# Performance work log

Hardware: AMD Instinct MI355X
Metric: run time of the kernel (lower is better)

Reference implementation:

```python
import jax, jax.numpy as jnp
import numpy as np

B, S, H, V, T, L = 32, 128, 1024, 32000, 100, 4
SD = 0.02


def setup_inputs() -> dict:
    key = jax.random.key(0)
    ks = jax.random.split(key, 20)
    f = jnp.float32
    return {
        "encoder_outputs": jax.random.normal(ks[0], (B, S, H), f),
        "encoder_hidden": jax.random.normal(ks[1], (L, B, H), f),
        "target_tensor": jax.random.randint(ks[2], (B, T), 0, V, dtype=jnp.int32),
        "emb": jax.random.normal(ks[3], (V, H), f) * SD,
        "w_ih0": jax.random.normal(ks[4], (3 * H, 2 * H), f) * SD,
        "w_hh0": jax.random.normal(ks[5], (3 * H, H), f) * SD,
        "b_ih0": jnp.zeros((3 * H,), f),
        "b_hh0": jnp.zeros((3 * H,), f),
        "w_ih": jax.random.normal(ks[6], (L - 1, 3 * H, H), f) * SD,
        "w_hh": jax.random.normal(ks[7], (L - 1, 3 * H, H), f) * SD,
        "b_ih": jnp.zeros((L - 1, 3 * H), f),
        "b_hh": jnp.zeros((L - 1, 3 * H), f),
        "out_w": jax.random.normal(ks[8], (V, H), f) * SD,
        "out_b": jnp.zeros((V,), f),
        "l1_w": jax.random.normal(ks[9], (3, 2 * H), f) * SD,
        "l1_b": jnp.zeros((3,), f),
        "l2_w": jax.random.normal(ks[10], (1, 3), f) * SD,
        "l2_b": jnp.zeros((1,), f),
    }


def _gru_cell(x, h, w_ih, w_hh, b_ih, b_hh):
    # PyTorch GRUCell math
    gi = x @ w_ih.T + b_ih          # [B, 3H]
    gh = h @ w_hh.T + b_hh          # [B, 3H]
    i_r, i_z, i_n = jnp.split(gi, 3, axis=-1)
    h_r, h_z, h_n = jnp.split(gh, 3, axis=-1)
    r = jax.nn.sigmoid(i_r + h_r)
    z = jax.nn.sigmoid(i_z + h_z)
    n = jnp.tanh(i_n + r * h_n)
    return (1.0 - z) * n + z * h


def reference(encoder_outputs, encoder_hidden, target_tensor, emb,
              w_ih0, w_hh0, b_ih0, b_hh0, w_ih, w_hh, b_ih, b_hh,
              out_w, out_b, l1_w, l1_b, l2_w, l2_b):
    b, h = encoder_hidden.shape[1], encoder_hidden.shape[2]
    enc_h = encoder_hidden[0]  # [B, H] 'updated_encoder_hidden'
    # teacher forcing: step 0 uses input 0, step i uses target[:, i-1]
    inputs = jnp.concatenate(
        [jnp.zeros((b, 1), target_tensor.dtype), target_tensor[:, :T - 1]],
        axis=1).T  # [T, B]

    def step(hidden, inp_t):
        # a[:] = hidden[0][-1] -> broadcast last batch row of layer-0 hidden
        a = jnp.broadcast_to(hidden[0, -1], (b, h))
        enc = jnp.concatenate([a, enc_h], axis=1)          # [B, 2H]
        s = (enc @ l1_w.T + l1_b) @ l2_w.T + l2_b          # [B, 1]
        scores = jax.nn.softmax(s, axis=0)                 # softmax over batch dim
        C = jnp.sum(enc_h * scores, axis=0)                # [H]
        e = jax.nn.relu(emb[inp_t])                        # [B, H]
        x = jnp.concatenate([e, jnp.broadcast_to(C, (b, h))], axis=-1)  # [B, 2H]
        h0 = _gru_cell(x, hidden[0], w_ih0, w_hh0, b_ih0, b_hh0)
        hs = [h0]
        xl = h0
        for l in range(L - 1):
            hl = _gru_cell(xl, hidden[l + 1], w_ih[l], w_hh[l], b_ih[l], b_hh[l])
            hs.append(hl)
            xl = hl
        logits = xl @ out_w.T + out_b                      # [B, V]
        return jnp.stack(hs), (logits, scores)

    hidden_fin, (logits, scores) = jax.lax.scan(step, encoder_hidden, inputs)
    dec_out = jax.nn.log_softmax(jnp.transpose(logits, (1, 0, 2)), axis=-1)  # [B, T, V]
    return dec_out, hidden_fin, scores[-1]
```

## Files before the change

### kernel.cpp

```cpp
#include <hip/hip_runtime.h>
#include <hip/hip_bf16.h>
#include <math.h>

#define B_ 32
#define H_ 1024
#define V_ 32000
#define T_ 100
#define L_ 4
#define TB_ (T_*B_)
#define N3H (3*H_)
#define NBLK 224
#define L0BLK 32
#define FSTRIDE 16
#define NVT (V_/128)

typedef __attribute__((ext_vector_type(8))) short bf16x8;
typedef __attribute__((ext_vector_type(4))) float f32x4;
typedef __attribute__((ext_vector_type(4))) unsigned short u16x4;
typedef __attribute__((ext_vector_type(8))) unsigned short u16x8;

__device__ inline unsigned short f2bf(float f) {
    union { float f; unsigned u; } v; v.f = f;
    unsigned r = v.u + 0x7fff + ((v.u >> 16) & 1);
    return (unsigned short)(r >> 16);
}
__device__ inline float bf2f(unsigned short u) {
    union { unsigned u; float f; } v; v.u = ((unsigned)u) << 16; return v.f;
}

__device__ inline bf16x8 ld_h16(const unsigned short* p) {
    union { unsigned long long u[2]; bf16x8 v; } r;
    r.u[0] = __hip_atomic_load((const unsigned long long*)p,
                               __ATOMIC_RELAXED, __HIP_MEMORY_SCOPE_AGENT);
    r.u[1] = __hip_atomic_load((const unsigned long long*)(p + 4),
                               __ATOMIC_RELAXED, __HIP_MEMORY_SCOPE_AGENT);
    return r.v;
}
__device__ inline void st_h2(unsigned short* p, unsigned short v) {
    __hip_atomic_store(p, v, __ATOMIC_RELAXED, __HIP_MEMORY_SCOPE_AGENT);
}

__device__ inline void gload_lds16(const unsigned short* g, unsigned short* lds)
{
    __builtin_amdgcn_global_load_lds(
        (const __attribute__((address_space(1))) void*)g,
        (__attribute__((address_space(3))) void*)lds, 16, 0, 0);
}

__global__ __launch_bounds__(256) void convbf_kernel(
    const float* __restrict__ src, unsigned short* __restrict__ dst, int n4)
{
    for (int i = blockIdx.x * 256 + threadIdx.x; i < n4; i += gridDim.x * 256) {
        float4 v = ((const float4*)src)[i];
        u16x4 o; o.x = f2bf(v.x); o.y = f2bf(v.y); o.z = f2bf(v.z); o.w = f2bf(v.w);
        ((u16x4*)dst)[i] = o;
    }
}

__global__ __launch_bounds__(256) void embed_bf_kernel(
    const int* __restrict__ target, const float* __restrict__ emb,
    unsigned short* __restrict__ Ebf)
{
    int bid = blockIdx.x;
    int t = bid >> 5, b = bid & 31;
    int tok = (t == 0) ? 0 : target[b * T_ + (t - 1)];
    float4 v = ((const float4*)(emb + (size_t)tok * H_))[threadIdx.x];
    u16x4 o;
    o.x = f2bf(fmaxf(v.x, 0.f)); o.y = f2bf(fmaxf(v.y, 0.f));
    o.z = f2bf(fmaxf(v.z, 0.f)); o.w = f2bf(fmaxf(v.w, 0.f));
    ((u16x4*)(Ebf + (size_t)bid * H_))[threadIdx.x] = o;
}

__global__ __launch_bounds__(256) void attn_pre_kernel(
    const float* __restrict__ enc_h, const float* __restrict__ l1_w,
    const float* __restrict__ l1_b, const float* __restrict__ l2_w,
    float* __restrict__ Cout, float* __restrict__ scores)
{
    __shared__ float L1h[96];
    __shared__ float sc[32];
    int tid = threadIdx.x, wv = tid >> 6, lane = tid & 63;
    for (int d = wv; d < 96; d += 4) {
        int b = d / 3, g = d - 3 * b;
        const float4* wp = (const float4*)(l1_w + (size_t)g * 2 * H_ + H_);
        const float4* ep = (const float4*)(enc_h + (size_t)b * H_);
        float s = 0.f;
        for (int q = lane; q < 256; q += 64) {
            float4 w4 = wp[q], e4 = ep[q];
            s += w4.x * e4.x + w4.y * e4.y + w4.z * e4.z + w4.w * e4.w;
        }
        for (int o = 32; o > 0; o >>= 1) s += __shfl_down(s, o);
        if (lane == 0) L1h[d] = s;
    }
    __syncthreads();
    if (tid < 32) {
        float cb = 0.f;
        for (int g = 0; g < 3; ++g) cb += l2_w[g] * (L1h[tid * 3 + g] + l1_b[g]);
        sc[tid] = cb;
    }
    __syncthreads();
    if (tid == 0) {
        float m = sc[0];
        for (int b = 1; b < 32; ++b) m = fmaxf(m, sc[b]);
        float s = 0.f;
        for (int b = 0; b < 32; ++b) { float e = expf(sc[b] - m); sc[b] = e; s += e; }
        float inv = 1.f / s;
        for (int b = 0; b < 32; ++b) { sc[b] *= inv; scores[b] = sc[b]; }
    }
    __syncthreads();
    float4 c = make_float4(0.f, 0.f, 0.f, 0.f);
    for (int b = 0; b < 32; ++b) {
        float4 e = ((const float4*)(enc_h + (size_t)b * H_))[tid];
        float ww = sc[b];
        c.x += ww * e.x; c.y += ww * e.y; c.z += ww * e.z; c.w += ww * e.w;
    }
    ((float4*)Cout)[tid] = c;
}

__global__ __launch_bounds__(256) void wcc_kernel(
    const float* __restrict__ w_ih0, const float* __restrict__ C,
    float* __restrict__ wcC)
{
    int row = blockIdx.x * 4 + (threadIdx.x >> 6);
    int lane = threadIdx.x & 63;
    const float4* wp = (const float4*)(w_ih0 + (size_t)row * 2 * H_ + H_);
    const float4* cp = (const float4*)C;
    float s = 0.f;
    for (int q = lane; q < 256; q += 64) {
        float4 w4 = wp[q], c4 = cp[q];
        s += w4.x * c4.x + w4.y * c4.y + w4.z * c4.z + w4.w * c4.w;
    }
    for (int o = 32; o > 0; o >>= 1) s += __shfl_down(s, o);
    if (lane == 0) wcC[row] = s;
}

__global__ __launch_bounds__(256) void gemm_staged(
    const unsigned short* __restrict__ A, int lda,
    const unsigned short* __restrict__ Bb,
    const float* __restrict__ bias, int M, int outMode,
    void* __restrict__ outp, float2* __restrict__ P)
{
    __shared__ unsigned short Wt[128 * 64];
    __shared__ unsigned short Ht[128 * 64];
    __shared__ float2 smp[4][4][16];

    const int tid = threadIdx.x, wv = tid >> 6, lane = tid & 63;
    const int rlo = lane & 15, khw = lane >> 4;
    const int rch = lane >> 3, slot = lane & 7;
    const int rowB = blockIdx.y * 128, colB = blockIdx.x * 128;
    const int wrow0 = rowB + (wv >> 1) * 64;
    const int wcol0 = colB + (wv & 1) * 64;
    const int rA = (wv >> 1) * 64, cA = (wv & 1) * 64;

    f32x4 acc[4][4];
    #pragma unroll
    for (int i = 0; i < 4; ++i)
        #pragma unroll
        for (int j = 0; j < 4; ++j) acc[i][j] = (f32x4){0.f, 0.f, 0.f, 0.f};

    for (int k0 = 0; k0 < H_; k0 += 64) {
        #pragma unroll
        for (int j = 0; j < 4; ++j) {
            int q = wv * 4 + j;
            int row = q * 8 + rch;
            int ss = slot ^ (row & 7);
            gload_lds16(A + (size_t)(rowB + row) * lda + k0 + ss * 8,
                        Wt + (size_t)q * 512);
            gload_lds16(Bb + (size_t)(colB + row) * H_ + k0 + ss * 8,
                        Ht + (size_t)q * 512);
        }
        __syncthreads();

        const char* WtB = (const char*)Wt;
        const char* HtB = (const char*)Ht;
        #pragma unroll
        for (int kk = 0; kk < 2; ++kk) {
            bf16x8 af[4], bfr[4];
            #pragma unroll
            for (int ri = 0; ri < 4; ++ri) {
                int row = rA + ri * 16 + rlo;
                int ch = (kk * 4 + khw) ^ (row & 7);
                af[ri] = *(const bf16x8*)(WtB + row * 128 + ch * 16);
            }
            #pragma unroll
            for (int ci = 0; ci < 4; ++ci) {
                int col = cA + ci * 16 + rlo;
                int ch = (kk * 4 + khw) ^ (col & 7);
                bfr[ci] = *(const bf16x8*)(HtB + col * 128 + ch * 16);
            }
            #pragma unroll
            for (int ri = 0; ri < 4; ++ri)
                #pragma unroll
                for (int ci = 0; ci < 4; ++ci)
                    acc[ri][ci] = __builtin_amdgcn_mfma_f32_16x16x32_bf16(
                        af[ri], bfr[ci], acc[ri][ci], 0, 0, 0);
        }
        __syncthreads();
    }

    int rowoff = (lane >> 4) * 4;
    if (outMode == 0) {
        #pragma unroll
        for (int ri = 0; ri < 4; ++ri) {
            int row = wrow0 + ri * 16 + rowoff;
            float4 bs = *(const float4*)(bias + row);
            #pragma unroll
            for (int ci = 0; ci < 4; ++ci) {
                int col = wcol0 + ci * 16 + rlo;
                u16x4 o;
                o.x = f2bf(acc[ri][ci][0] + bs.x); o.y = f2bf(acc[ri][ci][1] + bs.y);
                o.z = f2bf(acc[ri][ci][2] + bs.z); o.w = f2bf(acc[ri][ci][3] + bs.w);
                *(u16x4*)((unsigned short*)outp + (size_t)col * M + row) = o;
            }
        }
        return;
    }

    float cm[4], cs[4];
    #pragma unroll
    for (int ci = 0; ci < 4; ++ci) { cm[ci] = -INFINITY; cs[ci] = 0.f; }
    unsigned short* Lbf = (unsigned short*)outp;
    #pragma unroll
    for (int ri = 0; ri < 4; ++ri) {
        int row = wrow0 + ri * 16 + rowoff;
        float4 bs = *(const float4*)(bias + row);
        #pragma unroll
        for (int ci = 0; ci < 4; ++ci) {
            int col = wcol0 + ci * 16 + rlo;
            float4 v;
            v.x = acc[ri][ci][0] + bs.x; v.y = acc[ri][ci][1] + bs.y;
            v.z = acc[ri][ci][2] + bs.z; v.w = acc[ri][ci][3] + bs.w;
            u16x4 o; o.x = f2bf(v.x); o.y = f2bf(v.y);
            o.z = f2bf(v.z); o.w = f2bf(v.w);
            *(u16x4*)(Lbf + (size_t)col * V_ + row) = o;
            float m4 = fmaxf(fmaxf(v.x, v.y), fmaxf(v.z, v.w));
            if (m4 > cm[ci]) { cs[ci] *= __expf(cm[ci] - m4); cm[ci] = m4; }
            cs[ci] += __expf(v.x - cm[ci]) + __expf(v.y - cm[ci])
                    + __expf(v.z - cm[ci]) + __expf(v.w - cm[ci]);
        }
    }
    #pragma unroll
    for (int ci = 0; ci < 4; ++ci) {
        #pragma unroll
        for (int off = 16; off <= 32; off <<= 1) {
            float om = __shfl_xor(cm[ci], off);
            float os = __shfl_xor(cs[ci], off);
            float mm = fmaxf(cm[ci], om);
            cs[ci] = cs[ci] * __expf(cm[ci] - mm) + os * __expf(om - mm);
            cm[ci] = mm;
        }
        if ((lane >> 4) == 0) smp[wv][ci][rlo] = make_float2(cm[ci], cs[ci]);
    }
    __syncthreads();
    if (tid < 128) {
        int c = tid >> 6, ci = (tid >> 4) & 3, rl = tid & 15;
        float2 a = smp[c][ci][rl], b = smp[c + 2][ci][rl];
        float mm = fmaxf(a.x, b.x);
        float ss = a.y * __expf(a.x - mm) + b.y * __expf(b.x - mm);
        int col = colB + c * 64 + ci * 16 + rl;
        P[(size_t)blockIdx.y * TB_ + col] = make_float2(mm, ss);
    }
}

__global__ __launch_bounds__(256) void lse_finish_kernel(
    const float2* __restrict__ P, float* __restrict__ lse)
{
    int col = blockIdx.x * 256 + threadIdx.x;
    if (col >= TB_) return;
    float M = -INFINITY, S = 0.f;
    for (int i = 0; i < NVT; ++i) {
        float2 p = P[(size_t)i * TB_ + col];
        float mm = fmaxf(M, p.x);
        S = S * __expf(M - mm) + p.y * __expf(p.x - mm);
        M = mm;
    }
    lse[col] = M + logf(S);
}

__global__ __launch_bounds__(256) void subtract_kernel(
    const unsigned short* __restrict__ Lbf, const float* __restrict__ lse,
    float* __restrict__ dout)
{
    int col = blockIdx.x;
    int t = col >> 5, b = col & 31;
    float l = lse[col];
    const u16x8* L = (const u16x8*)(Lbf + (size_t)col * V_);
    float4* o = (float4*)(dout + ((size_t)b * T_ + t) * V_);
    for (int i = threadIdx.x; i < V_ / 8; i += 256) {
        u16x8 x = L[i];
        float4 v0, v1;
        v0.x = bf2f(x[0]) - l; v0.y = bf2f(x[1]) - l;
        v0.z = bf2f(x[2]) - l; v0.w = bf2f(x[3]) - l;
        v1.x = bf2f(x[4]) - l; v1.y = bf2f(x[5]) - l;
        v1.z = bf2f(x[6]) - l; v1.w = bf2f(x[7]) - l;
        o[i * 2] = v0; o[i * 2 + 1] = v1;
    }
}

__device__ inline void grid_bar4(unsigned* flags, unsigned round)
{
    __syncthreads();
    if (threadIdx.x == 0) {
        asm volatile("s_waitcnt vmcnt(0)" ::: "memory");
        __hip_atomic_store(&flags[(size_t)blockIdx.x * FSTRIDE], round,
                           __ATOMIC_RELAXED, __HIP_MEMORY_SCOPE_AGENT);
    }
    int ok = (threadIdx.x >= NBLK) ? 1 : 0;
    while (true) {
        if (!ok)
            ok = (__hip_atomic_load(&flags[(size_t)threadIdx.x * FSTRIDE],
                                    __ATOMIC_RELAXED, __HIP_MEMORY_SCOPE_AGENT) >= round);
        if (__syncthreads_and(ok)) break;
        __builtin_amdgcn_s_sleep(2);
    }
}

__global__ __launch_bounds__(512, 1) void decode_kernel(
    const unsigned short* __restrict__ whh0_bf,
    const unsigned short* __restrict__ wih_bf,
    const unsigned short* __restrict__ whh_bf,
    const unsigned short* __restrict__ G0,
    const float* __restrict__ b_ih0, const float* __restrict__ b_hh0,
    const float* __restrict__ b_ih,  const float* __restrict__ b_hh,
    const float* __restrict__ enc_hidden,
    unsigned short* __restrict__ hbf,
    unsigned short* __restrict__ Hist,
    float* __restrict__ hid_out,
    unsigned* __restrict__ flags)
{
    __shared__ float sacc[6][4][16][34];
    const int tid = threadIdx.x;
    const int wv = tid >> 6, lane = tid & 63;
    const int rlo = lane & 15, klane = (lane >> 4) * 8;
    const int rowoff = (lane >> 4) * 4;
    const int bid = blockIdx.x;

    int layer, f0;
    if (bid < L0BLK) { layer = 0; f0 = bid << 5; }
    else { int r = bid - L0BLK; layer = 1 + (r >> 6); f0 = (r & 63) << 4; }

    const unsigned short* Wih_l = (layer >= 1) ? wih_bf + (size_t)(layer - 1) * N3H * H_ : nullptr;
    const unsigned short* Whh_l = (layer >= 1) ? whh_bf + (size_t)(layer - 1) * N3H * H_ : whh0_bf;

    const int kc = wv & 3, srcgrp = wv >> 2;

    bf16x8 wreg[3][8];
    int rgv[3];
    #pragma unroll
    for (int i = 0; i < 3; ++i) {
        int rg = srcgrp * 3 + i;
        rgv[i] = rg;
        int wrow; const unsigned short* Wm;
        if (layer == 0)      { wrow = (rg >> 1) * H_ + f0 + (rg & 1) * 16; Wm = Whh_l; }
        else if (rg < 3)     { wrow = rg * H_ + f0;        Wm = Wih_l; }
        else                 { wrow = (rg - 3) * H_ + f0;  Wm = Whh_l; }
        const unsigned short* p = Wm + (size_t)(wrow + rlo) * H_ + kc * 256 + klane;
        #pragma unroll
        for (int s = 0; s < 8; ++s) wreg[i][s] = *(const bf16x8*)(p + s * 32);
    }
    #pragma unroll
    for (int i = 0; i < 3; ++i)
        #pragma unroll
        for (int s = 0; s < 8; ++s)
            asm volatile("" : "+v"(wreg[i][s]));

    const float* bihp = (layer == 0) ? b_ih0 : b_ih + (size_t)(layer - 1) * N3H;
    const float* bhhp = (layer == 0) ? b_hh0 : b_hh + (size_t)(layer - 1) * N3H;
    int jj, eb0;
    float hold0, hold1 = 0.f;
    if (layer == 0) {
        jj = f0 + (tid & 31);
        eb0 = tid >> 5;
        hold0 = enc_hidden[(size_t)eb0 * H_ + jj];
        hold1 = enc_hidden[(size_t)(eb0 + 16) * H_ + jj];
    } else {
        jj = f0 + (tid & 15);
        eb0 = tid >> 4;
        hold0 = enc_hidden[(size_t)layer * B_ * H_ + (size_t)eb0 * H_ + jj];
    }
    const float bir = bihp[jj], biz = bihp[H_ + jj], bin_ = bihp[2 * H_ + jj];
    const float bhr = bhhp[jj], bhz = bhhp[H_ + jj], bhn = bhhp[2 * H_ + jj];

    const size_t BH = (size_t)B_ * H_;

    for (int c = 0; c < T_ + L_ - 1; ++c) {
        int t = c - layer;
        if (t >= 0 && t < T_) {
            int pw = t & 1, pr = pw ^ 1;
            const unsigned short* hown  = hbf + ((size_t)pr * L_ + layer) * BH;
            const unsigned short* hprev = (layer > 0)
                ? hbf + ((size_t)pw * L_ + (layer - 1)) * BH : nullptr;

            f32x4 acc[3][2];
            #pragma unroll
            for (int i = 0; i < 3; ++i) {
                acc[i][0] = (f32x4){0.f, 0.f, 0.f, 0.f};
                acc[i][1] = (f32x4){0.f, 0.f, 0.f, 0.f};
            }

            const unsigned short* hsrc = (layer == 0 || srcgrp == 1) ? hown : hprev;
            const unsigned short* hp = hsrc + (size_t)rlo * H_ + kc * 256 + klane;
            #pragma unroll
            for (int s = 0; s < 8; ++s) {
                bf16x8 b0 = ld_h16(hp + s * 32);
                bf16x8 b1 = ld_h16(hp + 16 * H_ + s * 32);
                #pragma unroll
                for (int i = 0; i < 3; ++i) {
                    acc[i][0] = __builtin_amdgcn_mfma_f32_16x16x32_bf16(wreg[i][s], b0, acc[i][0], 0, 0, 0);
                    acc[i][1] = __builtin_amdgcn_mfma_f32_16x16x32_bf16(wreg[i][s], b1, acc[i][1], 0, 0, 0);
                }
            }

            #pragma unroll
            for (int i = 0; i < 3; ++i)
                #pragma unroll
                for (int r = 0; r < 4; ++r) {
                    sacc[rgv[i]][kc][rowoff + r][rlo]      = acc[i][0][r];
                    sacc[rgv[i]][kc][rowoff + r][16 + rlo] = acc[i][1][r];
                }
            __syncthreads();

            if (layer > 0) {
                int f = tid & 15, b = tid >> 4;
                float ir = bir, iz = biz, in_ = bin_;
                float hr = bhr, hz = bhz, hn = bhn;
                #pragma unroll
                for (int k2 = 0; k2 < 4; ++k2) {
                    ir += sacc[0][k2][f][b]; iz += sacc[1][k2][f][b]; in_ += sacc[2][k2][f][b];
                    hr += sacc[3][k2][f][b]; hz += sacc[4][k2][f][b]; hn += sacc[5][k2][f][b];
                }
                float r = 1.f / (1.f + expf(-(ir + hr)));
                float z = 1.f / (1.f + expf(-(iz + hz)));
                float n = tanhf(in_ + r * hn);
                float hnew = (1.f - z) * n + z * hold0;
                hold0 = hnew;
                unsigned short hb16 = f2bf(hnew);
                st_h2(&hbf[((size_t)pw * L_ + layer) * BH + (size_t)b * H_ + jj], hb16);
                if (layer == L_ - 1) Hist[((size_t)t * B_ + b) * H_ + jj] = hb16;
                if (t == T_ - 1) hid_out[(size_t)layer * BH + (size_t)b * H_ + jj] = hnew;
            } else {
                int fi = tid & 31;
                int rghalf = fi >> 4, fr = fi & 15;
                {
                    int b = eb0;
                    const unsigned short* g0p = G0 + ((size_t)t * B_ + b) * N3H;
                    float ir = bf2f(g0p[jj]) + bir;
                    float iz = bf2f(g0p[H_ + jj]) + biz;
                    float in_ = bf2f(g0p[2 * H_ + jj]) + bin_;
                    float hr = bhr, hz = bhz, hn = bhn;
                    #pragma unroll
                    for (int k2 = 0; k2 < 4; ++k2) {
                        hr += sacc[rghalf][k2][fr][b];
                        hz += sacc[2 + rghalf][k2][fr][b];
                        hn += sacc[4 + rghalf][k2][fr][b];
                    }
                    float r = 1.f / (1.f + expf(-(ir + hr)));
                    float z = 1.f / (1.f + expf(-(iz + hz)));
                    float n = tanhf(in_ + r * hn);
                    float hnew = (1.f - z) * n + z * hold0;
                    hold0 = hnew;
                    st_h2(&hbf[((size_t)pw * L_) * BH + (size_t)b * H_ + jj], f2bf(hnew));
                    if (t == T_ - 1) hid_out[(size_t)b * H_ + jj] = hnew;
                }
                {
                    int b = eb0 + 16;
                    const unsigned short* g0p = G0 + ((size_t)t * B_ + b) * N3H;
                    float ir = bf2f(g0p[jj]) + bir;
                    float iz = bf2f(g0p[H_ + jj]) + biz;
                    float in_ = bf2f(g0p[2 * H_ + jj]) + bin_;
                    float hr = bhr, hz = bhz, hn = bhn;
                    #pragma unroll
                    for (int k2 = 0; k2 < 4; ++k2) {
                        hr += sacc[rghalf][k2][fr][b];
                        hz += sacc[2 + rghalf][k2][fr][b];
                        hn += sacc[4 + rghalf][k2][fr][b];
                    }
                    float r = 1.f / (1.f + expf(-(ir + hr)));
                    float z = 1.f / (1.f + expf(-(iz + hz)));
                    float n = tanhf(in_ + r * hn);
                    float hnew = (1.f - z) * n + z * hold1;
                    hold1 = hnew;
                    st_h2(&hbf[((size_t)pw * L_) * BH + (size_t)b * H_ + jj], f2bf(hnew));
                    if (t == T_ - 1) hid_out[(size_t)b * H_ + jj] = hnew;
                }
            }
        }
        grid_bar4(flags, (unsigned)(c + 1));
    }
}

__global__ __launch_bounds__(256) void logsoftmax_kernel(float* __restrict__ dout)
{
    __shared__ float red[256];
    float4* x4 = (float4*)(dout + (size_t)blockIdx.x * V_);
    const int N4 = V_ / 4;
    int tid = threadIdx.x;

    float m = -INFINITY, s = 0.f;
    for (int i = tid; i < N4; i += 256) {
        float4 v = x4[i];
        float m4 = fmaxf(fmaxf(v.x, v.y), fmaxf(v.z, v.w));
        if (m4 > m) { s *= expf(m - m4); m = m4; }
        s += expf(v.x - m) + expf(v.y - m) + expf(v.z - m) + expf(v.w - m);
    }
    red[tid] = m; __syncthreads();
    for (int o = 128; o > 0; o >>= 1) {
        if (tid < o) red[tid] = fmaxf(red[tid], red[tid + o]);
        __syncthreads();
    }
    float M = red[0]; __syncthreads();
    red[tid] = s * expf(m - M); __syncthreads();
    for (int o = 128; o > 0; o >>= 1) {
        if (tid < o) red[tid] += red[tid + o];
        __syncthreads();
    }
    float lse = M + logf(red[0]);

    for (int i = tid; i < N4; i += 256) {
        float4 v = x4[i];
        v.x -= lse; v.y -= lse; v.z -= lse; v.w -= lse;
        x4[i] = v;
    }
}

__global__ __launch_bounds__(256) void gemm_logits_f32(
    const unsigned short* __restrict__ A,
    const unsigned short* __restrict__ Bb,
    const float* __restrict__ bias, float* __restrict__ dout)
{
    __shared__ unsigned short Wt[128 * 64];
    __shared__ unsigned short Ht[128 * 64];
    const int tid = threadIdx.x, wv = tid >> 6, lane = tid & 63;
    const int rlo = lane & 15, khw = lane >> 4;
    const int rch = lane >> 3, slot = lane & 7;
    const int rowB = blockIdx.y * 128, colB = blockIdx.x * 128;
    const int wrow0 = rowB + (wv >> 1) * 64;
    const int wcol0 = colB + (wv & 1) * 64;
    const int rA = (wv >> 1) * 64, cA = (wv & 1) * 64;

    f32x4 acc[4][4];
    #pragma unroll
    for (int i = 0; i < 4; ++i)
        #pragma unroll
        for (int j = 0; j < 4; ++j) acc[i][j] = (f32x4){0.f, 0.f, 0.f, 0.f};

    for (int k0 = 0; k0 < H_; k0 += 64) {
        #pragma unroll
        for (int j = 0; j < 4; ++j) {
            int q = wv * 4 + j;
            int row = q * 8 + rch;
            int ss = slot ^ (row & 7);
            gload_lds16(A + (size_t)(rowB + row) * H_ + k0 + ss * 8, Wt + (size_t)q * 512);
            gload_lds16(Bb + (size_t)(colB + row) * H_ + k0 + ss * 8, Ht + (size_t)q * 512);
        }
        __syncthreads();
        const char* WtB = (const char*)Wt;
        const char* HtB = (const char*)Ht;
        #pragma unroll
        for (int kk = 0; kk < 2; ++kk) {
            bf16x8 af[4], bfr[4];
            #pragma unroll
            for (int ri = 0; ri < 4; ++ri) {
                int row = rA + ri * 16 + rlo;
                int ch = (kk * 4 + khw) ^ (row & 7);
                af[ri] = *(const bf16x8*)(WtB + row * 128 + ch * 16);
            }
            #pragma unroll
            for (int ci = 0; ci < 4; ++ci) {
                int col = cA + ci * 16 + rlo;
                int ch = (kk * 4 + khw) ^ (col & 7);
                bfr[ci] = *(const bf16x8*)(HtB + col * 128 + ch * 16);
            }
            #pragma unroll
            for (int ri = 0; ri < 4; ++ri)
                #pragma unroll
                for (int ci = 0; ci < 4; ++ci)
                    acc[ri][ci] = __builtin_amdgcn_mfma_f32_16x16x32_bf16(
                        af[ri], bfr[ci], acc[ri][ci], 0, 0, 0);
        }
        __syncthreads();
    }
    int rowoff = (lane >> 4) * 4;
    #pragma unroll
    for (int ri = 0; ri < 4; ++ri) {
        int row = wrow0 + ri * 16 + rowoff;
        float4 bs = *(const float4*)(bias + row);
        #pragma unroll
        for (int ci = 0; ci < 4; ++ci) {
            int col = wcol0 + ci * 16 + rlo;
            int tt = col >> 5, b = col & 31;
            float4 v;
            v.x = acc[ri][ci][0] + bs.x; v.y = acc[ri][ci][1] + bs.y;
            v.z = acc[ri][ci][2] + bs.z; v.w = acc[ri][ci][3] + bs.w;
            *(float4*)(dout + ((size_t)b * T_ + tt) * V_ + row) = v;
        }
    }
}

extern "C" void kernel_launch(void* const* d_in, const int* in_sizes, int n_in,
                              void* d_out, int out_size, void* d_ws, size_t ws_size,
                              hipStream_t stream)
{
    (void)in_sizes; (void)n_in; (void)out_size;

    const float* enc_hidden = (const float*)d_in[1];
    const int*   target     = (const int*)  d_in[2];
    const float* emb        = (const float*)d_in[3];
    const float* w_ih0      = (const float*)d_in[4];
    const float* w_hh0      = (const float*)d_in[5];
    const float* b_ih0      = (const float*)d_in[6];
    const float* b_hh0      = (const float*)d_in[7];
    const float* w_ih       = (const float*)d_in[8];
    const float* w_hh       = (const float*)d_in[9];
    const float* b_ih       = (const float*)d_in[10];
    const float* b_hh       = (const float*)d_in[11];
    const float* out_w      = (const float*)d_in[12];
    const float* out_b      = (const float*)d_in[13];
    const float* l1_w       = (const float*)d_in[14];
    const float* l1_b       = (const float*)d_in[15];
    const float* l2_w       = (const float*)d_in[16];
    float* out = (float*)d_out;

    char* w = (char*)d_ws;
    auto alloc = [&](size_t bytes) -> char* {
        char* p = w; w += (bytes + 255) & ~(size_t)255; return p;
    };
    unsigned short* whh0_bf = (unsigned short*)alloc((size_t)N3H * H_ * 2);
    unsigned short* wih_bf  = (unsigned short*)alloc((size_t)3 * N3H * H_ * 2);
    unsigned short* whh_bf  = (unsigned short*)alloc((size_t)3 * N3H * H_ * 2);
    unsigned short* Ebf     = (unsigned short*)alloc((size_t)TB_ * H_ * 2);
    unsigned short* G0      = (unsigned short*)alloc((size_t)TB_ * N3H * 2);
    unsigned short* Hist    = (unsigned short*)alloc((size_t)TB_ * H_ * 2);
    unsigned short* hbf     = (unsigned short*)alloc((size_t)2 * L_ * B_ * H_ * 2);
    float*          Cbuf    = (float*)alloc(H_ * 4);
    float*          scores  = (float*)alloc(256);
    float*          wcC     = (float*)alloc(N3H * 4);
    unsigned*       flags   = (unsigned*)alloc((size_t)NBLK * FSTRIDE * 4);
    float2*         Ppart   = (float2*)alloc((size_t)NVT * TB_ * 8);
    float*          lse     = (float*)alloc((size_t)TB_ * 4);

    size_t used = (size_t)(w - (char*)d_ws);
    unsigned short* wih0f_bf = nullptr;
    if (used + (size_t)N3H * 2 * H_ * 2 + 256 <= ws_size)
        wih0f_bf = (unsigned short*)alloc((size_t)N3H * 2 * H_ * 2);
    used = (size_t)(w - (char*)d_ws);
    unsigned short* outw_bf = nullptr;
    if (used + (size_t)V_ * H_ * 2 + 256 <= ws_size)
        outw_bf = (unsigned short*)alloc((size_t)V_ * H_ * 2);
    used = (size_t)(w - (char*)d_ws);
    unsigned short* Lbf = nullptr;
    if (used + (size_t)TB_ * V_ * 2 + 256 <= ws_size)
        Lbf = (unsigned short*)alloc((size_t)TB_ * V_ * 2);

    const size_t LBH = (size_t)L_ * B_ * H_;

    hipMemsetAsync(flags, 0, (size_t)NBLK * FSTRIDE * 4, stream);

    convbf_kernel<<<512, 256, 0, stream>>>(w_hh0, whh0_bf, N3H * H_ / 4);
    convbf_kernel<<<1024, 256, 0, stream>>>(w_ih, wih_bf, 3 * N3H * H_ / 4);
    convbf_kernel<<<1024, 256, 0, stream>>>(w_hh, whh_bf, 3 * N3H * H_ / 4);
    if (wih0f_bf)
        convbf_kernel<<<1024, 256, 0, stream>>>(w_ih0, wih0f_bf, N3H * 2 * H_ / 4);
    if (outw_bf)
        convbf_kernel<<<2048, 256, 0, stream>>>(out_w, outw_bf, V_ * H_ / 4);
    embed_bf_kernel<<<TB_, 256, 0, stream>>>(target, emb, Ebf);
    convbf_kernel<<<128, 256, 0, stream>>>(enc_hidden, hbf + LBH, (int)(LBH / 4));
    attn_pre_kernel<<<1, 256, 0, stream>>>(enc_hidden, l1_w, l1_b, l2_w, Cbuf, scores);
    wcc_kernel<<<N3H / 4, 256, 0, stream>>>(w_ih0, Cbuf, wcC);

    gemm_staged<<<dim3(TB_ / 128, N3H / 128), 256, 0, stream>>>(
        wih0f_bf, 2 * H_, Ebf, wcC, N3H, 0, G0, nullptr);

    decode_kernel<<<NBLK, 512, 0, stream>>>(
        whh0_bf, wih_bf, whh_bf, G0, b_ih0, b_hh0, b_ih, b_hh,
        enc_hidden, hbf, Hist, out + (size_t)B_ * T_ * V_, flags);

    if (outw_bf && Lbf) {
        gemm_staged<<<dim3(TB_ / 128, V_ / 128), 256, 0, stream>>>(
            outw_bf, H_, Hist, out_b, V_, 2, Lbf, Ppart);
        lse_finish_kernel<<<(TB_ + 255) / 256, 256, 0, stream>>>(Ppart, lse);
        subtract_kernel<<<TB_, 256, 0, stream>>>(Lbf, lse, out);
    } else if (outw_bf) {
        gemm_logits_f32<<<dim3(TB_ / 128, V_ / 128), 256, 0, stream>>>(
            outw_bf, Hist, out_b, out);
        logsoftmax_kernel<<<TB_, 256, 0, stream>>>(out);
    }

    hipMemcpyAsync(out + (size_t)B_ * T_ * V_ + LBH, scores, B_ * 4,
                   hipMemcpyDeviceToDevice, stream);
}
```

Measured before the change: 1.821 ms.

## Overlap output-projection GEMM with recurrent decode using extra worker blocks

```diff
diff --git a/kernel.cpp b/kernel.cpp
--- a/kernel.cpp
+++ b/kernel.cpp
@@ -11,6 +11,8 @@
 #define N3H (3*H_)
 #define NBLK 224
 #define L0BLK 32
+#define NWRK 200
+#define NCT  25
 #define FSTRIDE 16
 #define NVT (V_/128)
 
@@ -38,6 +40,9 @@
 }
 __device__ inline void st_h2(unsigned short* p, unsigned short v) {
     __hip_atomic_store(p, v, __ATOMIC_RELAXED, __HIP_MEMORY_SCOPE_AGENT);
+}
+__device__ inline unsigned ld_flag(const unsigned* p) {
+    return __hip_atomic_load(p, __ATOMIC_RELAXED, __HIP_MEMORY_SCOPE_AGENT);
 }
 
 __device__ inline void gload_lds16(const unsigned short* g, unsigned short* lds)
@@ -136,12 +141,11 @@
 __global__ __launch_bounds__(256) void gemm_staged(
     const unsigned short* __restrict__ A, int lda,
     const unsigned short* __restrict__ Bb,
-    const float* __restrict__ bias, int M, int outMode,
-    void* __restrict__ outp, float2* __restrict__ P)
+    const float* __restrict__ bias, int M,
+    unsigned short* __restrict__ outp)
 {
     __shared__ unsigned short Wt[128 * 64];
     __shared__ unsigned short Ht[128 * 64];
-    __shared__ float2 smp[4][4][16];
 
     const int tid = threadIdx.x, wv = tid >> 6, lane = tid & 63;
     const int rlo = lane & 15, khw = lane >> 4;
@@ -198,27 +202,6 @@
     }
 
     int rowoff = (lane >> 4) * 4;
-    if (outMode == 0) {
-        #pragma unroll
-        for (int ri = 0; ri < 4; ++ri) {
-            int row = wrow0 + ri * 16 + rowoff;
-            float4 bs = *(const float4*)(bias + row);
-            #pragma unroll
-            for (int ci = 0; ci < 4; ++ci) {
-                int col = wcol0 + ci * 16 + rlo;
-                u16x4 o;
-                o.x = f2bf(acc[ri][ci][0] + bs.x); o.y = f2bf(acc[ri][ci][1] + bs.y);
-                o.z = f2bf(acc[ri][ci][2] + bs.z); o.w = f2bf(acc[ri][ci][3] + bs.w);
-                *(u16x4*)((unsigned short*)outp + (size_t)col * M + row) = o;
-            }
-        }
-        return;
-    }
-
-    float cm[4], cs[4];
-    #pragma unroll
-    for (int ci = 0; ci < 4; ++ci) { cm[ci] = -INFINITY; cs[ci] = 0.f; }
-    unsigned short* Lbf = (unsigned short*)outp;
     #pragma unroll
     for (int ri = 0; ri < 4; ++ri) {
         int row = wrow0 + ri * 16 + rowoff;
@@ -226,38 +209,11 @@
         #pragma unroll
         for (int ci = 0; ci < 4; ++ci) {
             int col = wcol0 + ci * 16 + rlo;
-            float4 v;
-            v.x = acc[ri][ci][0] + bs.x; v.y = acc[ri][ci][1] + bs.y;
-            v.z = acc[ri][ci][2] + bs.z; v.w = acc[ri][ci][3] + bs.w;
-            u16x4 o; o.x = f2bf(v.x); o.y = f2bf(v.y);
-            o.z = f2bf(v.z); o.w = f2bf(v.w);
-            *(u16x4*)(Lbf + (size_t)col * V_ + row) = o;
-            float m4 = fmaxf(fmaxf(v.x, v.y), fmaxf(v.z, v.w));
-            if (m4 > cm[ci]) { cs[ci] *= __expf(cm[ci] - m4); cm[ci] = m4; }
-            cs[ci] += __expf(v.x - cm[ci]) + __expf(v.y - cm[ci])
-                    + __expf(v.z - cm[ci]) + __expf(v.w - cm[ci]);
-        }
-    }
-    #pragma unroll
-    for (int ci = 0; ci < 4; ++ci) {
-        #pragma unroll
-        for (int off = 16; off <= 32; off <<= 1) {
-            float om = __shfl_xor(cm[ci], off);
-            float os = __shfl_xor(cs[ci], off);
-            float mm = fmaxf(cm[ci], om);
-            cs[ci] = cs[ci] * __expf(cm[ci] - mm) + os * __expf(om - mm);
-            cm[ci] = mm;
-        }
-        if ((lane >> 4) == 0) smp[wv][ci][rlo] = make_float2(cm[ci], cs[ci]);
-    }
-    __syncthreads();
-    if (tid < 128) {
-        int c = tid >> 6, ci = (tid >> 4) & 3, rl = tid & 15;
-        float2 a = smp[c][ci][rl], b = smp[c + 2][ci][rl];
-        float mm = fmaxf(a.x, b.x);
-        float ss = a.y * __expf(a.x - mm) + b.y * __expf(b.x - mm);
-        int col = colB + c * 64 + ci * 16 + rl;
-        P[(size_t)blockIdx.y * TB_ + col] = make_float2(mm, ss);
+            u16x4 o;
+            o.x = f2bf(acc[ri][ci][0] + bs.x); o.y = f2bf(acc[ri][ci][1] + bs.y);
+            o.z = f2bf(acc[ri][ci][2] + bs.z); o.w = f2bf(acc[ri][ci][3] + bs.w);
+            *(u16x4*)(outp + (size_t)col * M + row) = o;
+        }
     }
 }
 
@@ -314,7 +270,7 @@
     }
 }
 
-__global__ __launch_bounds__(512, 1) void decode_kernel(
+__global__ __launch_bounds__(512, 2) void decode_kernel(
     const unsigned short* __restrict__ whh0_bf,
     const unsigned short* __restrict__ wih_bf,
     const unsigned short* __restrict__ whh_bf,
@@ -325,14 +281,142 @@
     unsigned short* __restrict__ hbf,
     unsigned short* __restrict__ Hist,
     float* __restrict__ hid_out,
-    unsigned* __restrict__ flags)
-{
-    __shared__ float sacc[6][4][16][34];
+    unsigned* __restrict__ flags,
+    const unsigned short* __restrict__ outw,
+    const float* __restrict__ out_b,
+    unsigned short* __restrict__ Lbf,
+    float2* __restrict__ Ppart)
+{
+    alignas(16) __shared__ char smem[52224];
     const int tid = threadIdx.x;
+    const int bid = blockIdx.x;
     const int wv = tid >> 6, lane = tid & 63;
-    const int rlo = lane & 15, klane = (lane >> 4) * 8;
+    const int rlo = lane & 15;
     const int rowoff = (lane >> 4) * 4;
-    const int bid = blockIdx.x;
+
+    if (bid >= NBLK) {
+        unsigned short* Wt = (unsigned short*)smem;
+        unsigned short* Ht = (unsigned short*)(smem + 16384);
+        float2 (*smp)[4][16] = (float2 (*)[4][16])(smem + 32768);
+        const int wkr = bid - NBLK;
+        const int khw = lane >> 4;
+        const int rch = lane >> 3, slot = lane & 7;
+        const int rowq = wv >> 1, colh = wv & 1;
+        const int rA = rowq * 32, cA = colh * 64;
+
+        for (int ct = 0; ct < NCT; ++ct) {
+            unsigned need = (unsigned)(4 * ct + 7);
+            for (;;) {
+                int ok = 1;
+                if (tid < 64)
+                    ok = (ld_flag(&flags[(size_t)(160 + tid) * FSTRIDE]) >= need);
+                if (__syncthreads_and(ok)) break;
+                __builtin_amdgcn_s_sleep(32);
+            }
+            const int colB = ct * 128;
+            for (int rt = wkr; rt < NVT; rt += NWRK) {
+                const int rowB = rt * 128;
+                f32x4 acc[2][4];
+                #pragma unroll
+                for (int i = 0; i < 2; ++i)
+                    #pragma unroll
+                    for (int j = 0; j < 4; ++j) acc[i][j] = (f32x4){0.f, 0.f, 0.f, 0.f};
+
+                for (int k0 = 0; k0 < H_; k0 += 64) {
+                    #pragma unroll
+                    for (int j = 0; j < 2; ++j) {
+                        int q = wv * 2 + j;
+                        int row = q * 8 + rch;
+                        int ss = slot ^ (row & 7);
+                        gload_lds16(outw + (size_t)(rowB + row) * H_ + k0 + ss * 8,
+                                    Wt + (size_t)q * 512);
+                        bf16x8 hv = ld_h16(Hist + (size_t)(colB + row) * H_ + k0 + ss * 8);
+                        *(bf16x8*)(Ht + (size_t)row * 64 + slot * 8) = hv;
+                    }
+                    __syncthreads();
+                    const char* WtB = (const char*)Wt;
+                    const char* HtB = (const char*)Ht;
+                    #pragma unroll
+                    for (int kk = 0; kk < 2; ++kk) {
+                        bf16x8 af[2], bfr[4];
+                        #pragma unroll
+                        for (int ri = 0; ri < 2; ++ri) {
+                            int row = rA + ri * 16 + rlo;
+                            int ch = (kk * 4 + khw) ^ (row & 7);
+                            af[ri] = *(const bf16x8*)(WtB + row * 128 + ch * 16);
+                        }
+                        #pragma unroll
+                        for (int ci = 0; ci < 4; ++ci) {
+                            int col = cA + ci * 16 + rlo;
+                            int ch = (kk * 4 + khw) ^ (col & 7);
+                            bfr[ci] = *(const bf16x8*)(HtB + col * 128 + ch * 16);
+                        }
+                        #pragma unroll
+                        for (int ri = 0; ri < 2; ++ri)
+                            #pragma unroll
+                            for (int ci = 0; ci < 4; ++ci)
+                                acc[ri][ci] = __builtin_amdgcn_mfma_f32_16x16x32_bf16(
+                                    af[ri], bfr[ci], acc[ri][ci], 0, 0, 0);
+                    }
+                    __syncthreads();
+                }
+
+                float cm[4], cs[4];
+                #pragma unroll
+                for (int ci = 0; ci < 4; ++ci) { cm[ci] = -INFINITY; cs[ci] = 0.f; }
+                #pragma unroll
+                for (int ri = 0; ri < 2; ++ri) {
+                    int row = rowB + rA + ri * 16 + rowoff;
+                    float4 bs = *(const float4*)(out_b + row);
+                    #pragma unroll
+                    for (int ci = 0; ci < 4; ++ci) {
+                        int col = colB + cA + ci * 16 + rlo;
+                        float4 v;
+                        v.x = acc[ri][ci][0] + bs.x; v.y = acc[ri][ci][1] + bs.y;
+                        v.z = acc[ri][ci][2] + bs.z; v.w = acc[ri][ci][3] + bs.w;
+                        u16x4 o; o.x = f2bf(v.x); o.y = f2bf(v.y);
+                        o.z = f2bf(v.z); o.w = f2bf(v.w);
+                        *(u16x4*)(Lbf + (size_t)col * V_ + row) = o;
+                        float m4 = fmaxf(fmaxf(v.x, v.y), fmaxf(v.z, v.w));
+                        if (m4 > cm[ci]) { cs[ci] *= __expf(cm[ci] - m4); cm[ci] = m4; }
+                        cs[ci] += __expf(v.x - cm[ci]) + __expf(v.y - cm[ci])
+                                + __expf(v.z - cm[ci]) + __expf(v.w - cm[ci]);
+                    }
+                }
+                #pragma unroll
+                for (int ci = 0; ci < 4; ++ci) {
+                    #pragma unroll
+                    for (int off = 16; off <= 32; off <<= 1) {
+                        float om = __shfl_xor(cm[ci], off);
+                        float os = __shfl_xor(cs[ci], off);
+                        float mm = fmaxf(cm[ci], om);
+                        cs[ci] = cs[ci] * __expf(cm[ci] - mm) + os * __expf(om - mm);
+                        cm[ci] = mm;
+                    }
+                    if ((lane >> 4) == 0) smp[wv][ci][rlo] = make_float2(cm[ci], cs[ci]);
+                }
+                __syncthreads();
+                if (tid < 128) {
+                    int c2 = tid >> 6, ci = (tid >> 4) & 3, rl = tid & 15;
+                    float2 a = smp[c2][ci][rl];
+                    #pragma unroll
+                    for (int q = 1; q < 4; ++q) {
+                        float2 bq = smp[c2 + 2 * q][ci][rl];
+                        float mm = fmaxf(a.x, bq.x);
+                        a.y = a.y * __expf(a.x - mm) + bq.y * __expf(bq.x - mm);
+                        a.x = mm;
+                    }
+                    int col = colB + c2 * 64 + ci * 16 + rl;
+                    Ppart[(size_t)rt * TB_ + col] = a;
+                }
+                __syncthreads();
+            }
+        }
+        return;
+    }
+
+    float (*sacc)[4][16][34] = (float (*)[4][16][34])smem;
+    const int klane = (lane >> 4) * 8;
 
     int layer, f0;
     if (bid < L0BLK) { layer = 0; f0 = bid << 5; }
@@ -357,11 +441,6 @@
         #pragma unroll
         for (int s = 0; s < 8; ++s) wreg[i][s] = *(const bf16x8*)(p + s * 32);
     }
-    #pragma unroll
-    for (int i = 0; i < 3; ++i)
-        #pragma unroll
-        for (int s = 0; s < 8; ++s)
-            asm volatile("" : "+v"(wreg[i][s]));
 
     const float* bihp = (layer == 0) ? b_ih0 : b_ih + (size_t)(layer - 1) * N3H;
     const float* bhhp = (layer == 0) ? b_hh0 : b_hh + (size_t)(layer - 1) * N3H;
@@ -435,7 +514,7 @@
                 hold0 = hnew;
                 unsigned short hb16 = f2bf(hnew);
                 st_h2(&hbf[((size_t)pw * L_ + layer) * BH + (size_t)b * H_ + jj], hb16);
-                if (layer == L_ - 1) Hist[((size_t)t * B_ + b) * H_ + jj] = hb16;
+                if (layer == L_ - 1) st_h2(&Hist[((size_t)t * B_ + b) * H_ + jj], hb16);
                 if (t == T_ - 1) hid_out[(size_t)layer * BH + (size_t)b * H_ + jj] = hnew;
             } else {
                 int fi = tid & 31;
@@ -652,6 +731,7 @@
         Lbf = (unsigned short*)alloc((size_t)TB_ * V_ * 2);
 
     const size_t LBH = (size_t)L_ * B_ * H_;
+    const bool workers = (outw_bf != nullptr) && (Lbf != nullptr);
 
     hipMemsetAsync(flags, 0, (size_t)NBLK * FSTRIDE * 4, stream);
 
@@ -668,15 +748,14 @@
     wcc_kernel<<<N3H / 4, 256, 0, stream>>>(w_ih0, Cbuf, wcC);
 
     gemm_staged<<<dim3(TB_ / 128, N3H / 128), 256, 0, stream>>>(
-        wih0f_bf, 2 * H_, Ebf, wcC, N3H, 0, G0, nullptr);
-
-    decode_kernel<<<NBLK, 512, 0, stream>>>(
+        wih0f_bf, 2 * H_, Ebf, wcC, N3H, G0);
+
+    decode_kernel<<<workers ? NBLK + NWRK : NBLK, 512, 0, stream>>>(
         whh0_bf, wih_bf, whh_bf, G0, b_ih0, b_hh0, b_ih, b_hh,
-        enc_hidden, hbf, Hist, out + (size_t)B_ * T_ * V_, flags);
-
-    if (outw_bf && Lbf) {
-        gemm_staged<<<dim3(TB_ / 128, V_ / 128), 256, 0, stream>>>(
-            outw_bf, H_, Hist, out_b, V_, 2, Lbf, Ppart);
+        enc_hidden, hbf, Hist, out + (size_t)B_ * T_ * V_, flags,
+        outw_bf, out_b, Lbf, Ppart);
+
+    if (workers) {
         lse_finish_kernel<<<(TB_ + 255) / 256, 256, 0, stream>>>(Ppart, lse);
         subtract_kernel<<<TB_, 256, 0, stream>>>(Lbf, lse, out);
     } else if (outw_bf) {
```

Result: slower. 2.429 ms (+33.4%).

## Move persistent GRU weights from registers to LDS and global in decode kernel

Applied to the files above, without the earlier changes.

```diff
diff --git a/kernel.cpp b/kernel.cpp
--- a/kernel.cpp
+++ b/kernel.cpp
@@ -13,6 +13,9 @@
 #define L0BLK 32
 #define FSTRIDE 16
 #define NVT (V_/128)
+#define SACC_BYTES 52224
+#define LDSW_BYTES 98304
+#define DEC_SMEM (SACC_BYTES + LDSW_BYTES)
 
 typedef __attribute__((ext_vector_type(8))) short bf16x8;
 typedef __attribute__((ext_vector_type(4))) float f32x4;
@@ -327,7 +330,10 @@
     float* __restrict__ hid_out,
     unsigned* __restrict__ flags)
 {
-    __shared__ float sacc[6][4][16][34];
+    extern __shared__ char smem[];
+    float (*sacc)[4][16][34] = (float (*)[4][16][34])smem;
+    unsigned short* ldsw = (unsigned short*)(smem + SACC_BYTES);
+
     const int tid = threadIdx.x;
     const int wv = tid >> 6, lane = tid & 63;
     const int rlo = lane & 15, klane = (lane >> 4) * 8;
@@ -342,8 +348,11 @@
     const unsigned short* Whh_l = (layer >= 1) ? whh_bf + (size_t)(layer - 1) * N3H * H_ : whh0_bf;
 
     const int kc = wv & 3, srcgrp = wv >> 2;
-
-    bf16x8 wreg[3][8];
+    const bool useLds = (kc < 2);
+    const int lslot = srcgrp * 2 + kc;
+    unsigned short* lw = ldsw + (size_t)lslot * 12288;
+
+    const unsigned short* wp[3];
     int rgv[3];
     #pragma unroll
     for (int i = 0; i < 3; ++i) {
@@ -353,15 +362,17 @@
         if (layer == 0)      { wrow = (rg >> 1) * H_ + f0 + (rg & 1) * 16; Wm = Whh_l; }
         else if (rg < 3)     { wrow = rg * H_ + f0;        Wm = Wih_l; }
         else                 { wrow = (rg - 3) * H_ + f0;  Wm = Whh_l; }
-        const unsigned short* p = Wm + (size_t)(wrow + rlo) * H_ + kc * 256 + klane;
-        #pragma unroll
-        for (int s = 0; s < 8; ++s) wreg[i][s] = *(const bf16x8*)(p + s * 32);
-    }
-    #pragma unroll
-    for (int i = 0; i < 3; ++i)
-        #pragma unroll
-        for (int s = 0; s < 8; ++s)
-            asm volatile("" : "+v"(wreg[i][s]));
+        wp[i] = Wm + (size_t)(wrow + rlo) * H_ + kc * 256 + klane;
+    }
+    if (useLds) {
+        #pragma unroll
+        for (int i = 0; i < 3; ++i)
+            #pragma unroll
+            for (int s = 0; s < 8; ++s)
+                *(bf16x8*)(lw + ((i * 8 + s) * 64 + lane) * 8) =
+                    *(const bf16x8*)(wp[i] + s * 32);
+    }
+    __syncthreads();
 
     const float* bihp = (layer == 0) ? b_ih0 : b_ih + (size_t)(layer - 1) * N3H;
     const float* bhhp = (layer == 0) ? b_hh0 : b_hh + (size_t)(layer - 1) * N3H;
@@ -399,14 +410,29 @@
 
             const unsigned short* hsrc = (layer == 0 || srcgrp == 1) ? hown : hprev;
             const unsigned short* hp = hsrc + (size_t)rlo * H_ + kc * 256 + klane;
-            #pragma unroll
-            for (int s = 0; s < 8; ++s) {
-                bf16x8 b0 = ld_h16(hp + s * 32);
-                bf16x8 b1 = ld_h16(hp + 16 * H_ + s * 32);
+            if (useLds) {
                 #pragma unroll
-                for (int i = 0; i < 3; ++i) {
-                    acc[i][0] = __builtin_amdgcn_mfma_f32_16x16x32_bf16(wreg[i][s], b0, acc[i][0], 0, 0, 0);
-                    acc[i][1] = __builtin_amdgcn_mfma_f32_16x16x32_bf16(wreg[i][s], b1, acc[i][1], 0, 0, 0);
+                for (int s = 0; s < 8; ++s) {
+                    bf16x8 b0 = ld_h16(hp + s * 32);
+                    bf16x8 b1 = ld_h16(hp + 16 * H_ + s * 32);
+                    #pragma unroll
+                    for (int i = 0; i < 3; ++i) {
+                        bf16x8 a = *(const bf16x8*)(lw + ((i * 8 + s) * 64 + lane) * 8);
+                        acc[i][0] = __builtin_amdgcn_mfma_f32_16x16x32_bf16(a, b0, acc[i][0], 0, 0, 0);
+                        acc[i][1] = __builtin_amdgcn_mfma_f32_16x16x32_bf16(a, b1, acc[i][1], 0, 0, 0);
+                    }
+                }
+            } else {
+                #pragma unroll
+                for (int s = 0; s < 8; ++s) {
+                    bf16x8 b0 = ld_h16(hp + s * 32);
+                    bf16x8 b1 = ld_h16(hp + 16 * H_ + s * 32);
+                    #pragma unroll
+                    for (int i = 0; i < 3; ++i) {
+                        bf16x8 a = *(const bf16x8*)(wp[i] + s * 32);
+                        acc[i][0] = __builtin_amdgcn_mfma_f32_16x16x32_bf16(a, b0, acc[i][0], 0, 0, 0);
+                        acc[i][1] = __builtin_amdgcn_mfma_f32_16x16x32_bf16(a, b1, acc[i][1], 0, 0, 0);
+                    }
                 }
             }
 
@@ -670,7 +696,9 @@
     gemm_staged<<<dim3(TB_ / 128, N3H / 128), 256, 0, stream>>>(
         wih0f_bf, 2 * H_, Ebf, wcC, N3H, 0, G0, nullptr);
 
-    decode_kernel<<<NBLK, 512, 0, stream>>>(
+    hipFuncSetAttribute((const void*)decode_kernel,
+                        hipFuncAttributeMaxDynamicSharedMemorySize, DEC_SMEM);
+    decode_kernel<<<NBLK, 512, DEC_SMEM, stream>>>(
         whh0_bf, wih_bf, whh_bf, G0, b_ih0, b_hh0, b_ih, b_hh,
         enc_hidden, hbf, Hist, out + (size_t)B_ * T_ * V_, flags);
 
```

Result: slower. 2.182 ms (+19.8%).
